# Kernel optimization log

Hardware: AMD Instinct MI355X
Metric: run time of the kernel (lower is better)

Reference implementation:

```python
import jax, jax.numpy as jnp
import numpy as np

N = 50000      # nodes
E = 800000     # edges (avg degree 16)
D = 128        # hidden dim
L = 3          # message-passing layers
NU = 1         # DRew nu -> delay = max(k - nu, 0)


def setup_inputs() -> dict:
    key = jax.random.key(0)
    ks = jax.random.split(key, 6)
    x = jax.random.normal(ks[0], (N, D), dtype=jnp.float32)
    edge_index = jax.random.randint(ks[1], (2, E), 0, N)          # [2, E] (src, dst)
    edge_attr = jax.random.randint(ks[2], (E,), 1, L + 1)          # edge types in {1..L}
    scale = 1.0 / np.sqrt(D).astype(np.float32)
    Ws = jax.random.normal(ks[3], (L, D, D), dtype=jnp.float32) * scale       # mlp_s per layer
    bs = jnp.zeros((L, D), dtype=jnp.float32)
    Wk = jax.random.normal(ks[4], (L, L, D, D), dtype=jnp.float32) * scale    # mlp_k, padded; layer t uses k=1..t+1
    bk = jnp.zeros((L, L, D), dtype=jnp.float32)
    eps = jnp.zeros((L,), dtype=jnp.float32)
    return dict(x=x, edge_index=edge_index, edge_attr=edge_attr,
                Ws=Ws, bs=bs, Wk=Wk, bk=bk, eps=eps)


def reference(x, edge_index, edge_attr, Ws, bs, Wk, bk, eps):
    src, dst = edge_index[0], edge_index[1]
    xs = [x]
    for t in range(L):
        xt = xs[-1]
        # out = (1 + eps) * mlp_s(x)
        out = (1.0 + eps[t]) * jax.nn.relu(xt @ Ws[t] + bs[t])
        for k in range(1, t + 2):
            delay = max(k - NU, 0)
            x_src = xs[t - delay]                       # delayed node features
            mask = (edge_attr == k).astype(xt.dtype)    # edge-type mask (replaces boolean column select)
            msg = x_src[src] * mask[:, None]            # gather + mask: [E, D]
            agg = jax.ops.segment_sum(msg, dst, num_segments=N)  # scatter-add per destination
            out = out + jax.nn.relu(agg @ Wk[t, k - 1] + bk[t, k - 1])  # mlp_k(k)
        # gin_nn_post is an empty Sequential -> identity; then F.relu; then residual
        h = jax.nn.relu(out)
        xs.append(xt + h)
    return xs[-1]
```

## Files before the change

### kernel.cpp

```cpp
#include <hip/hip_runtime.h>
#include <hip/hip_bf16.h>


#define NODES 50000
#define EDGES 800000
#define DIM   128
#define ND    ((long)NODES * DIM)
#define NB3   (3 * NODES)
#define NPART 4
#define PSIZE (NODES / NPART)
#define NROWP 50048
#define NBLKS ((NB3 + 255) / 256)
#define NCELL 96
#define SORTN (NCELL * NBLKS)
#define FGRID ((SORTN + 255) / 256)

typedef __attribute__((ext_vector_type(8))) short  bf16x8;
typedef __attribute__((ext_vector_type(4))) float  f32x4;

#define LDS_STRIDE 136

__global__ __launch_bounds__(256) void init_kernel(
    const float* __restrict__ x, const float* __restrict__ Ws,
    const float* __restrict__ Wk, __hip_bfloat16* __restrict__ xb0,
    __hip_bfloat16* __restrict__ xb1, __hip_bfloat16* __restrict__ xb2,
    __hip_bfloat16* __restrict__ WT, int* __restrict__ cursor) {
  int b = blockIdx.x, tid = threadIdx.x;
  long i = (long)b * 256 + tid;
  if (i < ND / 4) {
    float4 v = ((const float4*)x)[i];
    union { __hip_bfloat16 h[4]; uint2 u; } pk;
    pk.h[0] = __float2bfloat16(v.x); pk.h[1] = __float2bfloat16(v.y);
    pk.h[2] = __float2bfloat16(v.z); pk.h[3] = __float2bfloat16(v.w);
    ((uint2*)xb0)[i] = pk.u;
  }
  if (b < 12) {
    const float* src = (b < 3) ? (Ws + (long)b * 16384) : (Wk + (long)(b - 3) * 16384);
    __hip_bfloat16* dst = WT + (long)b * 16384;
    for (int idx = tid; idx < 16384; idx += 256) {
      int k = idx >> 7, n = idx & 127;
      dst[n * 128 + k] = __float2bfloat16(src[idx]);
    }
  }
  if (b >= 12 && b < 12 + NBLKS) {
    int g = (b - 12) * 256 + tid;
    if (g < NB3) cursor[g] = 0;
  }
  if (b == 599 && tid < DIM) {
    xb0[(long)NODES * DIM + tid] = __float2bfloat16(0.f);
    xb1[(long)NODES * DIM + tid] = __float2bfloat16(0.f);
    xb2[(long)NODES * DIM + tid] = __float2bfloat16(0.f);
  }
}

__global__ __launch_bounds__(256) void hist_kernel(
    const int* __restrict__ ei, const int* __restrict__ attr,
    int* __restrict__ counts, int E) {
  int e = blockIdx.x * 256 + threadIdx.x;
  if (e >= E) return;
  atomicAdd(&counts[ei[E + e] * 3 + (attr[e] - 1)], 1);
}

__global__ __launch_bounds__(256) void scan_a_kernel(
    const int* __restrict__ counts, int* __restrict__ partial,
    int* __restrict__ blocksums, int n) {
  __shared__ int tmp[256];
  int gid = blockIdx.x * 256 + threadIdx.x;
  int v = (gid < n) ? ((counts[gid] + 3) & ~3) : 0;
  tmp[threadIdx.x] = v;
  __syncthreads();
  for (int off = 1; off < 256; off <<= 1) {
    int t = (threadIdx.x >= off) ? tmp[threadIdx.x - off] : 0;
    __syncthreads();
    tmp[threadIdx.x] += t;
    __syncthreads();
  }
  if (gid < n) partial[gid] = tmp[threadIdx.x] - v;
  if (threadIdx.x == 255) blocksums[blockIdx.x] = tmp[255];
}

__global__ __launch_bounds__(256) void scanc_bhist_kernel(
    int* __restrict__ rowptr, int* __restrict__ cursor,
    const int* __restrict__ blocksums, int* __restrict__ csr,
    int* __restrict__ G, int n) {
  __shared__ int h[NCELL];
  __shared__ int red[256];
  int tid = threadIdx.x;
  int partial = 0;
  for (int i = tid; i < blockIdx.x; i += 256) partial += blocksums[i];
  red[tid] = partial;
  if (tid < NCELL) h[tid] = 0;
  __syncthreads();
  for (int off = 128; off > 0; off >>= 1) {
    if (tid < off) red[tid] += red[tid + off];
    __syncthreads();
  }
  int bsoff = red[0];
  int gid = blockIdx.x * 256 + tid;
  if (gid < n) {
    int cnt = cursor[gid];
    int pcnt = (cnt + 3) & ~3;
    int val = rowptr[gid] + bsoff;
    rowptr[gid] = val;
    cursor[gid] = val;
    for (int i = cnt; i < pcnt; ++i) csr[val + i] = NODES;
    if (gid == n - 1) rowptr[n] = val + pcnt;
    int c = pcnt >> 2; if (c > 31) c = 31;
    int km1 = gid - (gid / 3) * 3;
    atomicAdd(&h[km1 * 32 + (31 - c)], 1);
  }
  __syncthreads();
  if (tid < NCELL) G[tid * NBLKS + blockIdx.x] = h[tid];
}

__global__ __launch_bounds__(256) void fill_kernel(
    const int* __restrict__ ei, const int* __restrict__ attr,
    int* __restrict__ cursor, int* __restrict__ csr_src, int E) {
  int p = blockIdx.x & (NPART - 1);
  int chunk = blockIdx.x >> 2;
  int e = chunk * 256 + threadIdx.x;
  if (e >= E) return;
  int d = ei[E + e];
  int lo = p * PSIZE;
  if (d < lo || d >= lo + PSIZE) return;
  int pos = atomicAdd(&cursor[d * 3 + (attr[e] - 1)], 1);
  csr_src[pos] = ei[e];
}

__global__ __launch_bounds__(256) void fscan_a_kernel(
    const int* __restrict__ in, int* __restrict__ partial,
    int* __restrict__ blocksums, int n) {
  __shared__ int tmp[256];
  int gid = blockIdx.x * 256 + threadIdx.x;
  int v = (gid < n) ? in[gid] : 0;
  tmp[threadIdx.x] = v;
  __syncthreads();
  for (int off = 1; off < 256; off <<= 1) {
    int t = (threadIdx.x >= off) ? tmp[threadIdx.x - off] : 0;
    __syncthreads();
    tmp[threadIdx.x] += t;
    __syncthreads();
  }
  if (gid < n) partial[gid] = tmp[threadIdx.x] - v;
  if (threadIdx.x == 255) blocksums[blockIdx.x] = tmp[255];
}

__global__ __launch_bounds__(256) void bfill_kernel(
    const int* __restrict__ rowptr, const int* __restrict__ G,
    const int* __restrict__ bsum2, int* __restrict__ wl, int nb2) {
  __shared__ int base[NCELL];
  __shared__ int ps[256];
  int tid = threadIdx.x;
  int v = (tid < nb2) ? bsum2[tid] : 0;
  ps[tid] = v;
  __syncthreads();
  for (int off = 1; off < 256; off <<= 1) {
    int t = (tid >= off) ? ps[tid - off] : 0;
    __syncthreads();
    ps[tid] += t;
    __syncthreads();
  }
  int incl = ps[tid];
  __syncthreads();
  ps[tid] = incl - v;
  __syncthreads();
  if (tid < NCELL) {
    int gidx = tid * NBLKS + blockIdx.x;
    base[tid] = G[gidx] + ps[gidx >> 8];
  }
  __syncthreads();
  int b = blockIdx.x * 256 + tid;
  if (b >= NB3) return;
  int pcnt = rowptr[b + 1] - rowptr[b];
  int c = pcnt >> 2; if (c > 31) c = 31;
  int km1 = b - (b / 3) * 3;
  int pos = atomicAdd(&base[km1 * 32 + (31 - c)], 1);
  wl[pos] = b;
}

__global__ __launch_bounds__(256, 6) void gather_kernel(
    const __hip_bfloat16* __restrict__ src,
    const int* __restrict__ rowptr, const int* __restrict__ csr,
    const int* __restrict__ wl,
    __hip_bfloat16* __restrict__ ag0, __hip_bfloat16* __restrict__ ag1,
    __hip_bfloat16* __restrict__ ag2, int nwork) {
  int group = (blockIdx.x * 256 + threadIdx.x) >> 4;
  int lane16 = threadIdx.x & 15;
  if (group >= nwork) return;
  int b = wl[group];
  int d = b / 3;
  int km1 = b - d * 3;
  __hip_bfloat16* ag = (km1 == 0) ? ag0 : ((km1 == 1) ? ag1 : ag2);
  int beg = rowptr[b], end = rowptr[b + 1];
  float a0 = 0.f, a1 = 0.f, a2 = 0.f, a3 = 0.f,
        a4 = 0.f, a5 = 0.f, a6 = 0.f, a7 = 0.f;
  for (int base = beg; base < end; base += 16) {
    int idxv = csr[base + lane16];
    int cnt = end - base; if (cnt > 16) cnt = 16;
    int q0 = __shfl(idxv, 0, 16);
    int q1 = __shfl(idxv, 1, 16);
    int q2 = __shfl(idxv, 2, 16);
    int q3 = __shfl(idxv, 3, 16);
    uint4 v0 = *(const uint4*)(src + (long)q0 * DIM + lane16 * 8);
    uint4 v1 = *(const uint4*)(src + (long)q1 * DIM + lane16 * 8);
    uint4 v2 = *(const uint4*)(src + (long)q2 * DIM + lane16 * 8);
    uint4 v3 = *(const uint4*)(src + (long)q3 * DIM + lane16 * 8);
    for (int j = 0; j < cnt; j += 4) {
      uint4 c0 = v0, c1 = v1, c2 = v2, c3 = v3;
      if (j + 4 < cnt) {
        q0 = __shfl(idxv, j + 4, 16);
        q1 = __shfl(idxv, j + 5, 16);
        q2 = __shfl(idxv, j + 6, 16);
        q3 = __shfl(idxv, j + 7, 16);
        v0 = *(const uint4*)(src + (long)q0 * DIM + lane16 * 8);
        v1 = *(const uint4*)(src + (long)q1 * DIM + lane16 * 8);
        v2 = *(const uint4*)(src + (long)q2 * DIM + lane16 * 8);
        v3 = *(const uint4*)(src + (long)q3 * DIM + lane16 * 8);
      }
      a0 += __uint_as_float(c0.x << 16) + __uint_as_float(c1.x << 16)
          + __uint_as_float(c2.x << 16) + __uint_as_float(c3.x << 16);
      a1 += __uint_as_float(c0.x & 0xffff0000u) + __uint_as_float(c1.x & 0xffff0000u)
          + __uint_as_float(c2.x & 0xffff0000u) + __uint_as_float(c3.x & 0xffff0000u);
      a2 += __uint_as_float(c0.y << 16) + __uint_as_float(c1.y << 16)
          + __uint_as_float(c2.y << 16) + __uint_as_float(c3.y << 16);
      a3 += __uint_as_float(c0.y & 0xffff0000u) + __uint_as_float(c1.y & 0xffff0000u)
          + __uint_as_float(c2.y & 0xffff0000u) + __uint_as_float(c3.y & 0xffff0000u);
      a4 += __uint_as_float(c0.z << 16) + __uint_as_float(c1.z << 16)
          + __uint_as_float(c2.z << 16) + __uint_as_float(c3.z << 16);
      a5 += __uint_as_float(c0.z & 0xffff0000u) + __uint_as_float(c1.z & 0xffff0000u)
          + __uint_as_float(c2.z & 0xffff0000u) + __uint_as_float(c3.z & 0xffff0000u);
      a6 += __uint_as_float(c0.w << 16) + __uint_as_float(c1.w << 16)
          + __uint_as_float(c2.w << 16) + __uint_as_float(c3.w << 16);
      a7 += __uint_as_float(c0.w & 0xffff0000u) + __uint_as_float(c1.w & 0xffff0000u)
          + __uint_as_float(c2.w & 0xffff0000u) + __uint_as_float(c3.w & 0xffff0000u);
    }
  }
  union { __hip_bfloat16 h[8]; uint4 u; } pk;
  pk.h[0] = __float2bfloat16(a0); pk.h[1] = __float2bfloat16(a1);
  pk.h[2] = __float2bfloat16(a2); pk.h[3] = __float2bfloat16(a3);
  pk.h[4] = __float2bfloat16(a4); pk.h[5] = __float2bfloat16(a5);
  pk.h[6] = __float2bfloat16(a6); pk.h[7] = __float2bfloat16(a7);
  *(uint4*)(ag + (long)d * DIM + lane16 * 8) = pk.u;
}

__global__ __launch_bounds__(256, 4) void lgemm_kernel(
    const __hip_bfloat16* __restrict__ xbSelf,
    const __hip_bfloat16* __restrict__ ag0,
    const __hip_bfloat16* __restrict__ ag1,
    const __hip_bfloat16* __restrict__ ag2,
    const __hip_bfloat16* __restrict__ WT,
    const float* __restrict__ bs_t,
    const float* __restrict__ bk_t,
    const float* __restrict__ epsp,
    __hip_bfloat16* __restrict__ xnb,
    float* __restrict__ xn,
    int t) {
  __shared__ __hip_bfloat16 b_lds[128 * LDS_STRIDE];

  int tid = threadIdx.x;
  long row0 = (long)blockIdx.x * 64;
  int wave = tid >> 6, lane = tid & 63;
  int l15 = lane & 15, q = lane >> 4;
  long arow = row0 + wave * 16 + l15;

  const __hip_bfloat16* Asrc[4] = {xbSelf, ag0, ag1, ag2};
  f32x4 out[8];

  for (int p = 0; p <= t + 1; ++p) {
    if (p > 0) __syncthreads();
    const __hip_bfloat16* Am = Asrc[p];
    uint4 af[4];
#pragma unroll
    for (int k0i = 0; k0i < 4; ++k0i)
      af[k0i] = *(const uint4*)(Am + arow * DIM + k0i * 32 + 8 * q);
    const __hip_bfloat16* W = (p == 0) ? (WT + (long)t * 16384)
                                       : (WT + (long)(3 + t * 3 + (p - 1)) * 16384);
    {
      const uint4* bq = (const uint4*)W;
#pragma unroll
      for (int i = 0; i < 8; ++i) {
        int idx = tid + 256 * i;
        int n = idx >> 4, k8 = idx & 15;
        uint4 v = bq[idx];
        *(uint4*)(b_lds + n * LDS_STRIDE + k8 * 8) = v;
      }
    }
    __syncthreads();

    f32x4 acc[8] = {};
#pragma unroll
    for (int k0i = 0; k0i < 4; ++k0i) {
      bf16x8 a = __builtin_bit_cast(bf16x8, af[k0i]);
#pragma unroll
      for (int j = 0; j < 8; ++j) {
        bf16x8 bfr = *(const bf16x8*)(b_lds + (16 * j + l15) * LDS_STRIDE + k0i * 32 + 8 * q);
        acc[j] = __builtin_amdgcn_mfma_f32_16x16x32_bf16(a, bfr, acc[j], 0, 0, 0);
      }
    }
    if (p == 0) {
      float sc = 1.0f + *epsp;
#pragma unroll
      for (int j = 0; j < 8; ++j) {
        float b = bs_t[16 * j + l15];
#pragma unroll
        for (int r = 0; r < 4; ++r) out[j][r] = sc * fmaxf(acc[j][r] + b, 0.f);
      }
    } else {
      const float* bb = bk_t + (p - 1) * 128;
#pragma unroll
      for (int j = 0; j < 8; ++j) {
        float b = bb[16 * j + l15];
#pragma unroll
        for (int r = 0; r < 4; ++r) out[j][r] += fmaxf(acc[j][r] + b, 0.f);
      }
    }
  }

  long rbase = row0 + wave * 16 + q * 4;
  bool fin = (xn != nullptr);
#pragma unroll
  for (int j = 0; j < 8; ++j) {
    int col = 16 * j + l15;
#pragma unroll
    for (int r = 0; r < 4; ++r) {
      long grow = rbase + r;
      if (grow < NODES) {
        float res = __bfloat162float(xbSelf[grow * DIM + col]);
        float v = res + fmaxf(out[j][r], 0.f);
        if (fin) xn[grow * DIM + col] = v;
        else     xnb[grow * DIM + col] = __float2bfloat16(v);
      }
    }
  }
}

extern "C" void kernel_launch(void* const* d_in, const int* in_sizes, int n_in,
                              void* d_out, int out_size, void* d_ws, size_t ws_size,
                              hipStream_t stream) {
  const float* x    = (const float*)d_in[0];
  const int*   ei   = (const int*)d_in[1];
  const int*   attr = (const int*)d_in[2];
  const float* Ws   = (const float*)d_in[3];
  const float* bs   = (const float*)d_in[4];
  const float* Wk   = (const float*)d_in[5];
  const float* bk   = (const float*)d_in[6];
  const float* eps  = (const float*)d_in[7];
  float* out = (float*)d_out;

  char* ws = (char*)d_ws;
  size_t off = 0;
  auto alloc = [&](size_t bytes) { char* p = ws + off; off += (bytes + 255) & ~(size_t)255; return p; };
  const size_t ROWB = (size_t)NROWP * DIM * 2;
  __hip_bfloat16* xb0  = (__hip_bfloat16*)alloc(ROWB);
  __hip_bfloat16* xb1  = (__hip_bfloat16*)alloc(ROWB);
  __hip_bfloat16* xb2  = (__hip_bfloat16*)alloc(ROWB);
  __hip_bfloat16* agA0 = (__hip_bfloat16*)alloc(ROWB);
  __hip_bfloat16* agA1 = (__hip_bfloat16*)alloc(ROWB);
  __hip_bfloat16* agA2 = (__hip_bfloat16*)alloc(ROWB);
  __hip_bfloat16* agB0 = (__hip_bfloat16*)alloc(ROWB);
  __hip_bfloat16* agB1 = (__hip_bfloat16*)alloc(ROWB);
  __hip_bfloat16* agC0 = (__hip_bfloat16*)alloc(ROWB);
  __hip_bfloat16* WT   = (__hip_bfloat16*)alloc(12 * 16384 * 2);
  int* cursor    = (int*)alloc((size_t)NB3 * 4);
  int* rowptr    = (int*)alloc((size_t)(NB3 + 1) * 4);
  int* blocksums = (int*)alloc(1024 * 4);
  int* G         = (int*)alloc((size_t)SORTN * 4);
  int* bsum2     = (int*)alloc(1024 * 4);
  int* wl        = (int*)alloc((size_t)NB3 * 4);
  int* csr_src   = (int*)alloc((size_t)(EDGES + 4 * NB3 + 16) * 4);

  int egrid  = (EDGES + 255) / 256;
  int igrid  = (int)(ND / 4 / 256);

  hipLaunchKernelGGL(init_kernel, dim3(igrid), dim3(256), 0, stream,
                     x, Ws, Wk, xb0, xb1, xb2, WT, cursor);
  hipLaunchKernelGGL(hist_kernel, dim3(egrid), dim3(256), 0, stream, ei, attr, cursor, EDGES);
  hipLaunchKernelGGL(scan_a_kernel, dim3(NBLKS), dim3(256), 0, stream, cursor, rowptr, blocksums, NB3);
  hipLaunchKernelGGL(scanc_bhist_kernel, dim3(NBLKS), dim3(256), 0, stream,
                     rowptr, cursor, blocksums, csr_src, G, NB3);
  hipLaunchKernelGGL(fill_kernel, dim3(egrid * NPART), dim3(256), 0, stream, ei, attr, cursor, csr_src, EDGES);
  hipLaunchKernelGGL(fscan_a_kernel, dim3(FGRID), dim3(256), 0, stream, G, G, bsum2, SORTN);
  hipLaunchKernelGGL(bfill_kernel, dim3(NBLKS), dim3(256), 0, stream, rowptr, G, bsum2, wl, FGRID);

  int ggrid = (NODES + 63) / 64;
  auto glaunch = [&](int nwork, const __hip_bfloat16* src, __hip_bfloat16* a0,
                     __hip_bfloat16* a1, __hip_bfloat16* a2) {
    int blocks = (nwork * 16 + 255) / 256;
    hipLaunchKernelGGL(gather_kernel, dim3(blocks), dim3(256), 0, stream,
                       src, rowptr, csr_src, wl, a0, a1, a2, nwork);
  };

  glaunch(3 * NODES, xb0, agA0, agA1, agA2);
  hipLaunchKernelGGL(lgemm_kernel, dim3(ggrid), dim3(256), 0, stream,
                     xb0, agA0, agA0, agA0, WT, bs + 0, bk + 0, eps + 0,
                     xb1, (float*)nullptr, 0);
  glaunch(2 * NODES, xb1, agB0, agB1, agB1);
  hipLaunchKernelGGL(lgemm_kernel, dim3(ggrid), dim3(256), 0, stream,
                     xb1, agB0, agA1, agA1, WT, bs + 128, bk + 3 * 128, eps + 1,
                     xb2, (float*)nullptr, 1);
  glaunch(NODES, xb2, agC0, agC0, agC0);
  hipLaunchKernelGGL(lgemm_kernel, dim3(ggrid), dim3(256), 0, stream,
                     xb2, agC0, agB1, agA2, WT, bs + 256, bk + 6 * 128, eps + 2,
                     (__hip_bfloat16*)nullptr, out, 2);
}
```

Measured before the change: 324.1 us.

## Fuse neighbor gather into per-layer GEMM kernel and drop degree-sorted worklist

The separate gather kernels and their bf16 aggregate buffers are removed. Each lgemm block now aggregates neighbor features for its own 64 rows straight into LDS before the MFMA step, reading from the delayed node buffers. The CSR is regrouped by edge type (type-major), and the degree-bucket worklist build (bucket histogram, scan, bfill) is dropped. This saves kernel launches and the write and re-read of six aggregate arrays. In exchange, load balance across rows of different degree is lost, layer 2 re-gathers type-2 and type-3 edges from xb0 that were previously precomputed in layer 0, and occupancy falls (launch bounds go from 4 to 3, plus extra LDS).

```diff
diff --git a/kernel.cpp b/kernel.cpp
--- a/kernel.cpp
+++ b/kernel.cpp
@@ -11,9 +11,6 @@
 #define PSIZE (NODES / NPART)
 #define NROWP 50048
 #define NBLKS ((NB3 + 255) / 256)
-#define NCELL 96
-#define SORTN (NCELL * NBLKS)
-#define FGRID ((SORTN + 255) / 256)
 
 typedef __attribute__((ext_vector_type(8))) short  bf16x8;
 typedef __attribute__((ext_vector_type(4))) float  f32x4;
@@ -58,7 +55,7 @@
     int* __restrict__ counts, int E) {
   int e = blockIdx.x * 256 + threadIdx.x;
   if (e >= E) return;
-  atomicAdd(&counts[ei[E + e] * 3 + (attr[e] - 1)], 1);
+  atomicAdd(&counts[(attr[e] - 1) * NODES + ei[E + e]], 1);
 }
 
 __global__ __launch_bounds__(256) void scan_a_kernel(
@@ -79,17 +76,14 @@
   if (threadIdx.x == 255) blocksums[blockIdx.x] = tmp[255];
 }
 
-__global__ __launch_bounds__(256) void scanc_bhist_kernel(
+__global__ __launch_bounds__(256) void scanc_kernel(
     int* __restrict__ rowptr, int* __restrict__ cursor,
-    const int* __restrict__ blocksums, int* __restrict__ csr,
-    int* __restrict__ G, int n) {
-  __shared__ int h[NCELL];
+    const int* __restrict__ blocksums, int* __restrict__ csr, int n) {
   __shared__ int red[256];
   int tid = threadIdx.x;
   int partial = 0;
   for (int i = tid; i < blockIdx.x; i += 256) partial += blocksums[i];
   red[tid] = partial;
-  if (tid < NCELL) h[tid] = 0;
   __syncthreads();
   for (int off = 128; off > 0; off >>= 1) {
     if (tid < off) red[tid] += red[tid + off];
@@ -105,12 +99,7 @@
     cursor[gid] = val;
     for (int i = cnt; i < pcnt; ++i) csr[val + i] = NODES;
     if (gid == n - 1) rowptr[n] = val + pcnt;
-    int c = pcnt >> 2; if (c > 31) c = 31;
-    int km1 = gid - (gid / 3) * 3;
-    atomicAdd(&h[km1 * 32 + (31 - c)], 1);
-  }
-  __syncthreads();
-  if (tid < NCELL) G[tid * NBLKS + blockIdx.x] = h[tid];
+  }
 }
 
 __global__ __launch_bounds__(256) void fill_kernel(
@@ -123,131 +112,16 @@
   int d = ei[E + e];
   int lo = p * PSIZE;
   if (d < lo || d >= lo + PSIZE) return;
-  int pos = atomicAdd(&cursor[d * 3 + (attr[e] - 1)], 1);
+  int pos = atomicAdd(&cursor[(attr[e] - 1) * NODES + d], 1);
   csr_src[pos] = ei[e];
 }
 
-__global__ __launch_bounds__(256) void fscan_a_kernel(
-    const int* __restrict__ in, int* __restrict__ partial,
-    int* __restrict__ blocksums, int n) {
-  __shared__ int tmp[256];
-  int gid = blockIdx.x * 256 + threadIdx.x;
-  int v = (gid < n) ? in[gid] : 0;
-  tmp[threadIdx.x] = v;
-  __syncthreads();
-  for (int off = 1; off < 256; off <<= 1) {
-    int t = (threadIdx.x >= off) ? tmp[threadIdx.x - off] : 0;
-    __syncthreads();
-    tmp[threadIdx.x] += t;
-    __syncthreads();
-  }
-  if (gid < n) partial[gid] = tmp[threadIdx.x] - v;
-  if (threadIdx.x == 255) blocksums[blockIdx.x] = tmp[255];
-}
-
-__global__ __launch_bounds__(256) void bfill_kernel(
-    const int* __restrict__ rowptr, const int* __restrict__ G,
-    const int* __restrict__ bsum2, int* __restrict__ wl, int nb2) {
-  __shared__ int base[NCELL];
-  __shared__ int ps[256];
-  int tid = threadIdx.x;
-  int v = (tid < nb2) ? bsum2[tid] : 0;
-  ps[tid] = v;
-  __syncthreads();
-  for (int off = 1; off < 256; off <<= 1) {
-    int t = (tid >= off) ? ps[tid - off] : 0;
-    __syncthreads();
-    ps[tid] += t;
-    __syncthreads();
-  }
-  int incl = ps[tid];
-  __syncthreads();
-  ps[tid] = incl - v;
-  __syncthreads();
-  if (tid < NCELL) {
-    int gidx = tid * NBLKS + blockIdx.x;
-    base[tid] = G[gidx] + ps[gidx >> 8];
-  }
-  __syncthreads();
-  int b = blockIdx.x * 256 + tid;
-  if (b >= NB3) return;
-  int pcnt = rowptr[b + 1] - rowptr[b];
-  int c = pcnt >> 2; if (c > 31) c = 31;
-  int km1 = b - (b / 3) * 3;
-  int pos = atomicAdd(&base[km1 * 32 + (31 - c)], 1);
-  wl[pos] = b;
-}
-
-__global__ __launch_bounds__(256, 6) void gather_kernel(
-    const __hip_bfloat16* __restrict__ src,
+__global__ __launch_bounds__(256, 3) void lgemm_kernel(
+    const __hip_bfloat16* __restrict__ xbSelf,
+    const __hip_bfloat16* __restrict__ g1,
+    const __hip_bfloat16* __restrict__ g2,
+    const __hip_bfloat16* __restrict__ g3,
     const int* __restrict__ rowptr, const int* __restrict__ csr,
-    const int* __restrict__ wl,
-    __hip_bfloat16* __restrict__ ag0, __hip_bfloat16* __restrict__ ag1,
-    __hip_bfloat16* __restrict__ ag2, int nwork) {
-  int group = (blockIdx.x * 256 + threadIdx.x) >> 4;
-  int lane16 = threadIdx.x & 15;
-  if (group >= nwork) return;
-  int b = wl[group];
-  int d = b / 3;
-  int km1 = b - d * 3;
-  __hip_bfloat16* ag = (km1 == 0) ? ag0 : ((km1 == 1) ? ag1 : ag2);
-  int beg = rowptr[b], end = rowptr[b + 1];
-  float a0 = 0.f, a1 = 0.f, a2 = 0.f, a3 = 0.f,
-        a4 = 0.f, a5 = 0.f, a6 = 0.f, a7 = 0.f;
-  for (int base = beg; base < end; base += 16) {
-    int idxv = csr[base + lane16];
-    int cnt = end - base; if (cnt > 16) cnt = 16;
-    int q0 = __shfl(idxv, 0, 16);
-    int q1 = __shfl(idxv, 1, 16);
-    int q2 = __shfl(idxv, 2, 16);
-    int q3 = __shfl(idxv, 3, 16);
-    uint4 v0 = *(const uint4*)(src + (long)q0 * DIM + lane16 * 8);
-    uint4 v1 = *(const uint4*)(src + (long)q1 * DIM + lane16 * 8);
-    uint4 v2 = *(const uint4*)(src + (long)q2 * DIM + lane16 * 8);
-    uint4 v3 = *(const uint4*)(src + (long)q3 * DIM + lane16 * 8);
-    for (int j = 0; j < cnt; j += 4) {
-      uint4 c0 = v0, c1 = v1, c2 = v2, c3 = v3;
-      if (j + 4 < cnt) {
-        q0 = __shfl(idxv, j + 4, 16);
-        q1 = __shfl(idxv, j + 5, 16);
-        q2 = __shfl(idxv, j + 6, 16);
-        q3 = __shfl(idxv, j + 7, 16);
-        v0 = *(const uint4*)(src + (long)q0 * DIM + lane16 * 8);
-        v1 = *(const uint4*)(src + (long)q1 * DIM + lane16 * 8);
-        v2 = *(const uint4*)(src + (long)q2 * DIM + lane16 * 8);
-        v3 = *(const uint4*)(src + (long)q3 * DIM + lane16 * 8);
-      }
-      a0 += __uint_as_float(c0.x << 16) + __uint_as_float(c1.x << 16)
-          + __uint_as_float(c2.x << 16) + __uint_as_float(c3.x << 16);
-      a1 += __uint_as_float(c0.x & 0xffff0000u) + __uint_as_float(c1.x & 0xffff0000u)
-          + __uint_as_float(c2.x & 0xffff0000u) + __uint_as_float(c3.x & 0xffff0000u);
-      a2 += __uint_as_float(c0.y << 16) + __uint_as_float(c1.y << 16)
-          + __uint_as_float(c2.y << 16) + __uint_as_float(c3.y << 16);
-      a3 += __uint_as_float(c0.y & 0xffff0000u) + __uint_as_float(c1.y & 0xffff0000u)
-          + __uint_as_float(c2.y & 0xffff0000u) + __uint_as_float(c3.y & 0xffff0000u);
-      a4 += __uint_as_float(c0.z << 16) + __uint_as_float(c1.z << 16)
-          + __uint_as_float(c2.z << 16) + __uint_as_float(c3.z << 16);
-      a5 += __uint_as_float(c0.z & 0xffff0000u) + __uint_as_float(c1.z & 0xffff0000u)
-          + __uint_as_float(c2.z & 0xffff0000u) + __uint_as_float(c3.z & 0xffff0000u);
-      a6 += __uint_as_float(c0.w << 16) + __uint_as_float(c1.w << 16)
-          + __uint_as_float(c2.w << 16) + __uint_as_float(c3.w << 16);
-      a7 += __uint_as_float(c0.w & 0xffff0000u) + __uint_as_float(c1.w & 0xffff0000u)
-          + __uint_as_float(c2.w & 0xffff0000u) + __uint_as_float(c3.w & 0xffff0000u);
-    }
-  }
-  union { __hip_bfloat16 h[8]; uint4 u; } pk;
-  pk.h[0] = __float2bfloat16(a0); pk.h[1] = __float2bfloat16(a1);
-  pk.h[2] = __float2bfloat16(a2); pk.h[3] = __float2bfloat16(a3);
-  pk.h[4] = __float2bfloat16(a4); pk.h[5] = __float2bfloat16(a5);
-  pk.h[6] = __float2bfloat16(a6); pk.h[7] = __float2bfloat16(a7);
-  *(uint4*)(ag + (long)d * DIM + lane16 * 8) = pk.u;
-}
-
-__global__ __launch_bounds__(256, 4) void lgemm_kernel(
-    const __hip_bfloat16* __restrict__ xbSelf,
-    const __hip_bfloat16* __restrict__ ag0,
-    const __hip_bfloat16* __restrict__ ag1,
-    const __hip_bfloat16* __restrict__ ag2,
     const __hip_bfloat16* __restrict__ WT,
     const float* __restrict__ bs_t,
     const float* __restrict__ bk_t,
@@ -256,6 +130,7 @@
     float* __restrict__ xn,
     int t) {
   __shared__ __hip_bfloat16 b_lds[128 * LDS_STRIDE];
+  __shared__ __hip_bfloat16 a_lds[64 * LDS_STRIDE];
 
   int tid = threadIdx.x;
   long row0 = (long)blockIdx.x * 64;
@@ -263,27 +138,97 @@
   int l15 = lane & 15, q = lane >> 4;
   long arow = row0 + wave * 16 + l15;
 
-  const __hip_bfloat16* Asrc[4] = {xbSelf, ag0, ag1, ag2};
+  const __hip_bfloat16* gsrc[3] = {g1, g2, g3};
   f32x4 out[8];
 
   for (int p = 0; p <= t + 1; ++p) {
-    if (p > 0) __syncthreads();
-    const __hip_bfloat16* Am = Asrc[p];
-    uint4 af[4];
-#pragma unroll
-    for (int k0i = 0; k0i < 4; ++k0i)
-      af[k0i] = *(const uint4*)(Am + arow * DIM + k0i * 32 + 8 * q);
     const __hip_bfloat16* W = (p == 0) ? (WT + (long)t * 16384)
                                        : (WT + (long)(3 + t * 3 + (p - 1)) * 16384);
-    {
-      const uint4* bq = (const uint4*)W;
-#pragma unroll
-      for (int i = 0; i < 8; ++i) {
-        int idx = tid + 256 * i;
-        int n = idx >> 4, k8 = idx & 15;
-        uint4 v = bq[idx];
-        *(uint4*)(b_lds + n * LDS_STRIDE + k8 * 8) = v;
-      }
+    const uint4* bq = (const uint4*)W;
+    uint4 wst[8];
+#pragma unroll
+    for (int i = 0; i < 8; ++i) wst[i] = bq[tid + 256 * i];
+
+    if (p > 0) __syncthreads();
+
+    uint4 af[4];
+    if (p == 0) {
+#pragma unroll
+      for (int k0i = 0; k0i < 4; ++k0i)
+        af[k0i] = *(const uint4*)(xbSelf + arow * DIM + k0i * 32 + 8 * q);
+    } else {
+      const __hip_bfloat16* S = gsrc[p - 1];
+      int km1 = p - 1;
+      int nl = (int)row0 + wave * 16 + (lane < 16 ? lane : 16);
+      if (nl > NODES) nl = NODES;
+      int rp = rowptr[km1 * NODES + nl];
+#pragma unroll
+      for (int s = 0; s < 4; ++s) {
+        int rowl = q * 4 + s;
+        int beg = __shfl(rp, rowl, 64);
+        int end = __shfl(rp, rowl + 1, 64);
+        float a0 = 0.f, a1 = 0.f, a2 = 0.f, a3 = 0.f,
+              a4 = 0.f, a5 = 0.f, a6 = 0.f, a7 = 0.f;
+        for (int base = beg; base < end; base += 16) {
+          int idxv = csr[base + l15];
+          int cnt = end - base; if (cnt > 16) cnt = 16;
+          int q0 = __shfl(idxv, 0, 16);
+          int q1 = __shfl(idxv, 1, 16);
+          int q2 = __shfl(idxv, 2, 16);
+          int q3 = __shfl(idxv, 3, 16);
+          uint4 v0 = *(const uint4*)(S + (long)q0 * DIM + l15 * 8);
+          uint4 v1 = *(const uint4*)(S + (long)q1 * DIM + l15 * 8);
+          uint4 v2 = *(const uint4*)(S + (long)q2 * DIM + l15 * 8);
+          uint4 v3 = *(const uint4*)(S + (long)q3 * DIM + l15 * 8);
+          for (int j = 0; j < cnt; j += 4) {
+            uint4 c0 = v0, c1 = v1, c2 = v2, c3 = v3;
+            if (j + 4 < cnt) {
+              q0 = __shfl(idxv, j + 4, 16);
+              q1 = __shfl(idxv, j + 5, 16);
+              q2 = __shfl(idxv, j + 6, 16);
+              q3 = __shfl(idxv, j + 7, 16);
+              v0 = *(const uint4*)(S + (long)q0 * DIM + l15 * 8);
+              v1 = *(const uint4*)(S + (long)q1 * DIM + l15 * 8);
+              v2 = *(const uint4*)(S + (long)q2 * DIM + l15 * 8);
+              v3 = *(const uint4*)(S + (long)q3 * DIM + l15 * 8);
+            }
+            a0 += __uint_as_float(c0.x << 16) + __uint_as_float(c1.x << 16)
+                + __uint_as_float(c2.x << 16) + __uint_as_float(c3.x << 16);
+            a1 += __uint_as_float(c0.x & 0xffff0000u) + __uint_as_float(c1.x & 0xffff0000u)
+                + __uint_as_float(c2.x & 0xffff0000u) + __uint_as_float(c3.x & 0xffff0000u);
+            a2 += __uint_as_float(c0.y << 16) + __uint_as_float(c1.y << 16)
+                + __uint_as_float(c2.y << 16) + __uint_as_float(c3.y << 16);
+            a3 += __uint_as_float(c0.y & 0xffff0000u) + __uint_as_float(c1.y & 0xffff0000u)
+                + __uint_as_float(c2.y & 0xffff0000u) + __uint_as_float(c3.y & 0xffff0000u);
+            a4 += __uint_as_float(c0.z << 16) + __uint_as_float(c1.z << 16)
+                + __uint_as_float(c2.z << 16) + __uint_as_float(c3.z << 16);
+            a5 += __uint_as_float(c0.z & 0xffff0000u) + __uint_as_float(c1.z & 0xffff0000u)
+                + __uint_as_float(c2.z & 0xffff0000u) + __uint_as_float(c3.z & 0xffff0000u);
+            a6 += __uint_as_float(c0.w << 16) + __uint_as_float(c1.w << 16)
+                + __uint_as_float(c2.w << 16) + __uint_as_float(c3.w << 16);
+            a7 += __uint_as_float(c0.w & 0xffff0000u) + __uint_as_float(c1.w & 0xffff0000u)
+                + __uint_as_float(c2.w & 0xffff0000u) + __uint_as_float(c3.w & 0xffff0000u);
+          }
+        }
+        union { __hip_bfloat16 h[8]; uint4 u; } pk;
+        pk.h[0] = __float2bfloat16(a0); pk.h[1] = __float2bfloat16(a1);
+        pk.h[2] = __float2bfloat16(a2); pk.h[3] = __float2bfloat16(a3);
+        pk.h[4] = __float2bfloat16(a4); pk.h[5] = __float2bfloat16(a5);
+        pk.h[6] = __float2bfloat16(a6); pk.h[7] = __float2bfloat16(a7);
+        *(uint4*)(a_lds + (wave * 16 + rowl) * LDS_STRIDE + l15 * 8) = pk.u;
+      }
+    }
+
+#pragma unroll
+    for (int i = 0; i < 8; ++i) {
+      int idx = tid + 256 * i;
+      int n = idx >> 4, k8 = idx & 15;
+      *(uint4*)(b_lds + n * LDS_STRIDE + k8 * 8) = wst[i];
+    }
+    if (p > 0) {
+#pragma unroll
+      for (int k0i = 0; k0i < 4; ++k0i)
+        af[k0i] = *(const uint4*)(a_lds + (wave * 16 + l15) * LDS_STRIDE + k0i * 32 + 8 * q);
     }
     __syncthreads();
 
@@ -354,20 +299,11 @@
   __hip_bfloat16* xb0  = (__hip_bfloat16*)alloc(ROWB);
   __hip_bfloat16* xb1  = (__hip_bfloat16*)alloc(ROWB);
   __hip_bfloat16* xb2  = (__hip_bfloat16*)alloc(ROWB);
-  __hip_bfloat16* agA0 = (__hip_bfloat16*)alloc(ROWB);
-  __hip_bfloat16* agA1 = (__hip_bfloat16*)alloc(ROWB);
-  __hip_bfloat16* agA2 = (__hip_bfloat16*)alloc(ROWB);
-  __hip_bfloat16* agB0 = (__hip_bfloat16*)alloc(ROWB);
-  __hip_bfloat16* agB1 = (__hip_bfloat16*)alloc(ROWB);
-  __hip_bfloat16* agC0 = (__hip_bfloat16*)alloc(ROWB);
   __hip_bfloat16* WT   = (__hip_bfloat16*)alloc(12 * 16384 * 2);
   int* cursor    = (int*)alloc((size_t)NB3 * 4);
-  int* rowptr    = (int*)alloc((size_t)(NB3 + 1) * 4);
+  int* rowptr    = (int*)alloc((size_t)(NB3 + 1) * 4 + 256);
   int* blocksums = (int*)alloc(1024 * 4);
-  int* G         = (int*)alloc((size_t)SORTN * 4);
-  int* bsum2     = (int*)alloc(1024 * 4);
-  int* wl        = (int*)alloc((size_t)NB3 * 4);
-  int* csr_src   = (int*)alloc((size_t)(EDGES + 4 * NB3 + 16) * 4);
+  int* csr_src   = (int*)alloc((size_t)(EDGES + 4 * NB3 + 64) * 4);
 
   int egrid  = (EDGES + 255) / 256;
   int igrid  = (int)(ND / 4 / 256);
@@ -376,30 +312,21 @@
                      x, Ws, Wk, xb0, xb1, xb2, WT, cursor);
   hipLaunchKernelGGL(hist_kernel, dim3(egrid), dim3(256), 0, stream, ei, attr, cursor, EDGES);
   hipLaunchKernelGGL(scan_a_kernel, dim3(NBLKS), dim3(256), 0, stream, cursor, rowptr, blocksums, NB3);
-  hipLaunchKernelGGL(scanc_bhist_kernel, dim3(NBLKS), dim3(256), 0, stream,
-                     rowptr, cursor, blocksums, csr_src, G, NB3);
+  hipLaunchKernelGGL(scanc_kernel, dim3(NBLKS), dim3(256), 0, stream,
+                     rowptr, cursor, blocksums, csr_src, NB3);
   hipLaunchKernelGGL(fill_kernel, dim3(egrid * NPART), dim3(256), 0, stream, ei, attr, cursor, csr_src, EDGES);
-  hipLaunchKernelGGL(fscan_a_kernel, dim3(FGRID), dim3(256), 0, stream, G, G, bsum2, SORTN);
-  hipLaunchKernelGGL(bfill_kernel, dim3(NBLKS), dim3(256), 0, stream, rowptr, G, bsum2, wl, FGRID);
 
   int ggrid = (NODES + 63) / 64;
-  auto glaunch = [&](int nwork, const __hip_bfloat16* src, __hip_bfloat16* a0,
-                     __hip_bfloat16* a1, __hip_bfloat16* a2) {
-    int blocks = (nwork * 16 + 255) / 256;
-    hipLaunchKernelGGL(gather_kernel, dim3(blocks), dim3(256), 0, stream,
-                       src, rowptr, csr_src, wl, a0, a1, a2, nwork);
-  };
-
-  glaunch(3 * NODES, xb0, agA0, agA1, agA2);
   hipLaunchKernelGGL(lgemm_kernel, dim3(ggrid), dim3(256), 0, stream,
-                     xb0, agA0, agA0, agA0, WT, bs + 0, bk + 0, eps + 0,
+                     xb0, xb0, (const __hip_bfloat16*)nullptr, (const __hip_bfloat16*)nullptr,
+                     rowptr, csr_src, WT, bs + 0, bk + 0, eps + 0,
                      xb1, (float*)nullptr, 0);
-  glaunch(2 * NODES, xb1, agB0, agB1, agB1);
   hipLaunchKernelGGL(lgemm_kernel, dim3(ggrid), dim3(256), 0, stream,
-                     xb1, agB0, agA1, agA1, WT, bs + 128, bk + 3 * 128, eps + 1,
+                     xb1, xb1, xb0, (const __hip_bfloat16*)nullptr,
+                     rowptr, csr_src, WT, bs + 128, bk + 3 * 128, eps + 1,
                      xb2, (float*)nullptr, 1);
-  glaunch(NODES, xb2, agC0, agC0, agC0);
   hipLaunchKernelGGL(lgemm_kernel, dim3(ggrid), dim3(256), 0, stream,
-                     xb2, agC0, agB1, agA2, WT, bs + 256, bk + 6 * 128, eps + 2,
+                     xb2, xb2, xb1, xb0,
+                     rowptr, csr_src, WT, bs + 256, bk + 6 * 128, eps + 2,
                      (__hip_bfloat16*)nullptr, out, 2);
 }
```

After: 417.3 us. 28.7% more time.

## Fuse CSR build into one cooperative kernel, drop degree-sorted worklist, type-major layout

Applied to the files above, without the earlier changes.

Merges init, histogram, scan, offset fixup and fill into a single cooperative kernel with grid.sync barriers, replacing seven launches. The degree-bucketed worklist (bucket histogram, scan, bfill) is removed, and the bucket index moves from node-major (d*3+k) to type-major (k*NODES+d), so gather groups map directly to buckets. This cuts launch and sync overhead and preprocessing work. In exchange the gather loses degree-balanced scheduling and the build runs on a fixed grid of 1024 blocks with grid-wide barriers.

```diff
diff --git a/kernel.cpp b/kernel.cpp
--- a/kernel.cpp
+++ b/kernel.cpp
@@ -1,5 +1,8 @@
 #include <hip/hip_runtime.h>
 #include <hip/hip_bf16.h>
+#include <hip/hip_cooperative_groups.h>
+
+namespace cg = cooperative_groups;
 
 
 #define NODES 50000
@@ -11,187 +14,120 @@
 #define PSIZE (NODES / NPART)
 #define NROWP 50048
 #define NBLKS ((NB3 + 255) / 256)
-#define NCELL 96
-#define SORTN (NCELL * NBLKS)
-#define FGRID ((SORTN + 255) / 256)
+#define EGRID ((EDGES + 255) / 256)
 
 typedef __attribute__((ext_vector_type(8))) short  bf16x8;
 typedef __attribute__((ext_vector_type(4))) float  f32x4;
 
 #define LDS_STRIDE 136
 
-__global__ __launch_bounds__(256) void init_kernel(
+__global__ __launch_bounds__(256, 4) void build_kernel(
     const float* __restrict__ x, const float* __restrict__ Ws,
     const float* __restrict__ Wk, __hip_bfloat16* __restrict__ xb0,
     __hip_bfloat16* __restrict__ xb1, __hip_bfloat16* __restrict__ xb2,
-    __hip_bfloat16* __restrict__ WT, int* __restrict__ cursor) {
-  int b = blockIdx.x, tid = threadIdx.x;
-  long i = (long)b * 256 + tid;
-  if (i < ND / 4) {
+    __hip_bfloat16* __restrict__ WT, int* __restrict__ cursor,
+    const int* __restrict__ ei, const int* __restrict__ attr,
+    int* __restrict__ rowptr, int* __restrict__ blocksums,
+    int* __restrict__ csr) {
+  cg::grid_group grid = cg::this_grid();
+  __shared__ int tmp[256];
+  __shared__ int red[256];
+
+  const int tid = threadIdx.x;
+  const int gtid = blockIdx.x * 256 + tid;
+  const int nth = gridDim.x * 256;
+
+  for (int i = gtid; i < (int)(ND / 4); i += nth) {
     float4 v = ((const float4*)x)[i];
     union { __hip_bfloat16 h[4]; uint2 u; } pk;
     pk.h[0] = __float2bfloat16(v.x); pk.h[1] = __float2bfloat16(v.y);
     pk.h[2] = __float2bfloat16(v.z); pk.h[3] = __float2bfloat16(v.w);
     ((uint2*)xb0)[i] = pk.u;
   }
-  if (b < 12) {
-    const float* src = (b < 3) ? (Ws + (long)b * 16384) : (Wk + (long)(b - 3) * 16384);
-    __hip_bfloat16* dst = WT + (long)b * 16384;
-    for (int idx = tid; idx < 16384; idx += 256) {
-      int k = idx >> 7, n = idx & 127;
-      dst[n * 128 + k] = __float2bfloat16(src[idx]);
-    }
-  }
-  if (b >= 12 && b < 12 + NBLKS) {
-    int g = (b - 12) * 256 + tid;
-    if (g < NB3) cursor[g] = 0;
-  }
-  if (b == 599 && tid < DIM) {
-    xb0[(long)NODES * DIM + tid] = __float2bfloat16(0.f);
-    xb1[(long)NODES * DIM + tid] = __float2bfloat16(0.f);
-    xb2[(long)NODES * DIM + tid] = __float2bfloat16(0.f);
-  }
-}
-
-__global__ __launch_bounds__(256) void hist_kernel(
-    const int* __restrict__ ei, const int* __restrict__ attr,
-    int* __restrict__ counts, int E) {
-  int e = blockIdx.x * 256 + threadIdx.x;
-  if (e >= E) return;
-  atomicAdd(&counts[ei[E + e] * 3 + (attr[e] - 1)], 1);
-}
-
-__global__ __launch_bounds__(256) void scan_a_kernel(
-    const int* __restrict__ counts, int* __restrict__ partial,
-    int* __restrict__ blocksums, int n) {
-  __shared__ int tmp[256];
-  int gid = blockIdx.x * 256 + threadIdx.x;
-  int v = (gid < n) ? ((counts[gid] + 3) & ~3) : 0;
-  tmp[threadIdx.x] = v;
-  __syncthreads();
-  for (int off = 1; off < 256; off <<= 1) {
-    int t = (threadIdx.x >= off) ? tmp[threadIdx.x - off] : 0;
+  for (int idx = gtid; idx < 12 * 16384; idx += nth) {
+    int wb = idx >> 14, r = idx & 16383;
+    int k = r >> 7, n = r & 127;
+    const float* src = (wb < 3) ? (Ws + (long)wb * 16384) : (Wk + (long)(wb - 3) * 16384);
+    WT[(long)wb * 16384 + n * 128 + k] = __float2bfloat16(src[r]);
+  }
+  for (int g = gtid; g < NB3; g += nth) cursor[g] = 0;
+  if (gtid < 3 * DIM) {
+    int which = gtid >> 7, dcol = gtid & 127;
+    __hip_bfloat16* xb = (which == 0) ? xb0 : ((which == 1) ? xb1 : xb2);
+    xb[(long)NODES * DIM + dcol] = __float2bfloat16(0.f);
+  }
+  grid.sync();
+
+  for (int e = gtid; e < EDGES; e += nth)
+    atomicAdd(&cursor[(attr[e] - 1) * NODES + ei[EDGES + e]], 1);
+  grid.sync();
+
+  if (blockIdx.x < NBLKS) {
+    int gid = blockIdx.x * 256 + tid;
+    int v = (gid < NB3) ? ((cursor[gid] + 3) & ~3) : 0;
+    tmp[tid] = v;
     __syncthreads();
-    tmp[threadIdx.x] += t;
+    for (int off = 1; off < 256; off <<= 1) {
+      int t = (tid >= off) ? tmp[tid - off] : 0;
+      __syncthreads();
+      tmp[tid] += t;
+      __syncthreads();
+    }
+    if (gid < NB3) rowptr[gid] = tmp[tid] - v;
+    if (tid == 255) blocksums[blockIdx.x] = tmp[255];
+  }
+  grid.sync();
+
+  if (blockIdx.x < NBLKS) {
+    int partial = 0;
+    for (int i = tid; i < (int)blockIdx.x; i += 256) partial += blocksums[i];
+    red[tid] = partial;
     __syncthreads();
-  }
-  if (gid < n) partial[gid] = tmp[threadIdx.x] - v;
-  if (threadIdx.x == 255) blocksums[blockIdx.x] = tmp[255];
-}
-
-__global__ __launch_bounds__(256) void scanc_bhist_kernel(
-    int* __restrict__ rowptr, int* __restrict__ cursor,
-    const int* __restrict__ blocksums, int* __restrict__ csr,
-    int* __restrict__ G, int n) {
-  __shared__ int h[NCELL];
-  __shared__ int red[256];
-  int tid = threadIdx.x;
-  int partial = 0;
-  for (int i = tid; i < blockIdx.x; i += 256) partial += blocksums[i];
-  red[tid] = partial;
-  if (tid < NCELL) h[tid] = 0;
-  __syncthreads();
-  for (int off = 128; off > 0; off >>= 1) {
-    if (tid < off) red[tid] += red[tid + off];
-    __syncthreads();
-  }
-  int bsoff = red[0];
-  int gid = blockIdx.x * 256 + tid;
-  if (gid < n) {
-    int cnt = cursor[gid];
-    int pcnt = (cnt + 3) & ~3;
-    int val = rowptr[gid] + bsoff;
-    rowptr[gid] = val;
-    cursor[gid] = val;
-    for (int i = cnt; i < pcnt; ++i) csr[val + i] = NODES;
-    if (gid == n - 1) rowptr[n] = val + pcnt;
-    int c = pcnt >> 2; if (c > 31) c = 31;
-    int km1 = gid - (gid / 3) * 3;
-    atomicAdd(&h[km1 * 32 + (31 - c)], 1);
-  }
-  __syncthreads();
-  if (tid < NCELL) G[tid * NBLKS + blockIdx.x] = h[tid];
-}
-
-__global__ __launch_bounds__(256) void fill_kernel(
-    const int* __restrict__ ei, const int* __restrict__ attr,
-    int* __restrict__ cursor, int* __restrict__ csr_src, int E) {
-  int p = blockIdx.x & (NPART - 1);
-  int chunk = blockIdx.x >> 2;
-  int e = chunk * 256 + threadIdx.x;
-  if (e >= E) return;
-  int d = ei[E + e];
-  int lo = p * PSIZE;
-  if (d < lo || d >= lo + PSIZE) return;
-  int pos = atomicAdd(&cursor[d * 3 + (attr[e] - 1)], 1);
-  csr_src[pos] = ei[e];
-}
-
-__global__ __launch_bounds__(256) void fscan_a_kernel(
-    const int* __restrict__ in, int* __restrict__ partial,
-    int* __restrict__ blocksums, int n) {
-  __shared__ int tmp[256];
-  int gid = blockIdx.x * 256 + threadIdx.x;
-  int v = (gid < n) ? in[gid] : 0;
-  tmp[threadIdx.x] = v;
-  __syncthreads();
-  for (int off = 1; off < 256; off <<= 1) {
-    int t = (threadIdx.x >= off) ? tmp[threadIdx.x - off] : 0;
-    __syncthreads();
-    tmp[threadIdx.x] += t;
-    __syncthreads();
-  }
-  if (gid < n) partial[gid] = tmp[threadIdx.x] - v;
-  if (threadIdx.x == 255) blocksums[blockIdx.x] = tmp[255];
-}
-
-__global__ __launch_bounds__(256) void bfill_kernel(
-    const int* __restrict__ rowptr, const int* __restrict__ G,
-    const int* __restrict__ bsum2, int* __restrict__ wl, int nb2) {
-  __shared__ int base[NCELL];
-  __shared__ int ps[256];
-  int tid = threadIdx.x;
-  int v = (tid < nb2) ? bsum2[tid] : 0;
-  ps[tid] = v;
-  __syncthreads();
-  for (int off = 1; off < 256; off <<= 1) {
-    int t = (tid >= off) ? ps[tid - off] : 0;
-    __syncthreads();
-    ps[tid] += t;
-    __syncthreads();
-  }
-  int incl = ps[tid];
-  __syncthreads();
-  ps[tid] = incl - v;
-  __syncthreads();
-  if (tid < NCELL) {
-    int gidx = tid * NBLKS + blockIdx.x;
-    base[tid] = G[gidx] + ps[gidx >> 8];
-  }
-  __syncthreads();
-  int b = blockIdx.x * 256 + tid;
-  if (b >= NB3) return;
-  int pcnt = rowptr[b + 1] - rowptr[b];
-  int c = pcnt >> 2; if (c > 31) c = 31;
-  int km1 = b - (b / 3) * 3;
-  int pos = atomicAdd(&base[km1 * 32 + (31 - c)], 1);
-  wl[pos] = b;
+    for (int off = 128; off > 0; off >>= 1) {
+      if (tid < off) red[tid] += red[tid + off];
+      __syncthreads();
+    }
+    int bsoff = red[0];
+    int gid = blockIdx.x * 256 + tid;
+    if (gid < NB3) {
+      int cnt = cursor[gid];
+      int pcnt = (cnt + 3) & ~3;
+      int val = rowptr[gid] + bsoff;
+      rowptr[gid] = val;
+      cursor[gid] = val;
+      for (int i = cnt; i < pcnt; ++i) csr[val + i] = NODES;
+      if (gid == NB3 - 1) rowptr[NB3] = val + pcnt;
+    }
+  }
+  grid.sync();
+
+  for (int vb = blockIdx.x; vb < EGRID * NPART; vb += gridDim.x) {
+    int p = vb & (NPART - 1);
+    int chunk = vb >> 2;
+    int e = chunk * 256 + tid;
+    if (e < EDGES) {
+      int d = ei[EDGES + e];
+      int lo = p * PSIZE;
+      if (d >= lo && d < lo + PSIZE) {
+        int pos = atomicAdd(&cursor[(attr[e] - 1) * NODES + d], 1);
+        csr[pos] = ei[e];
+      }
+    }
+  }
 }
 
 __global__ __launch_bounds__(256, 6) void gather_kernel(
     const __hip_bfloat16* __restrict__ src,
     const int* __restrict__ rowptr, const int* __restrict__ csr,
-    const int* __restrict__ wl,
     __hip_bfloat16* __restrict__ ag0, __hip_bfloat16* __restrict__ ag1,
     __hip_bfloat16* __restrict__ ag2, int nwork) {
   int group = (blockIdx.x * 256 + threadIdx.x) >> 4;
   int lane16 = threadIdx.x & 15;
   if (group >= nwork) return;
-  int b = wl[group];
-  int d = b / 3;
-  int km1 = b - d * 3;
+  int km1 = (group >= 2 * NODES) ? 2 : ((group >= NODES) ? 1 : 0);
+  int d = group - km1 * NODES;
   __hip_bfloat16* ag = (km1 == 0) ? ag0 : ((km1 == 1) ? ag1 : ag2);
-  int beg = rowptr[b], end = rowptr[b + 1];
+  int beg = rowptr[group], end = rowptr[group + 1];
   float a0 = 0.f, a1 = 0.f, a2 = 0.f, a3 = 0.f,
         a4 = 0.f, a5 = 0.f, a6 = 0.f, a7 = 0.f;
   for (int base = beg; base < end; base += 16) {
@@ -362,33 +298,26 @@
   __hip_bfloat16* agC0 = (__hip_bfloat16*)alloc(ROWB);
   __hip_bfloat16* WT   = (__hip_bfloat16*)alloc(12 * 16384 * 2);
   int* cursor    = (int*)alloc((size_t)NB3 * 4);
-  int* rowptr    = (int*)alloc((size_t)(NB3 + 1) * 4);
+  int* rowptr    = (int*)alloc((size_t)(NB3 + 1) * 4 + 256);
   int* blocksums = (int*)alloc(1024 * 4);
-  int* G         = (int*)alloc((size_t)SORTN * 4);
-  int* bsum2     = (int*)alloc(1024 * 4);
-  int* wl        = (int*)alloc((size_t)NB3 * 4);
-  int* csr_src   = (int*)alloc((size_t)(EDGES + 4 * NB3 + 16) * 4);
-
-  int egrid  = (EDGES + 255) / 256;
-  int igrid  = (int)(ND / 4 / 256);
-
-  hipLaunchKernelGGL(init_kernel, dim3(igrid), dim3(256), 0, stream,
-                     x, Ws, Wk, xb0, xb1, xb2, WT, cursor);
-  hipLaunchKernelGGL(hist_kernel, dim3(egrid), dim3(256), 0, stream, ei, attr, cursor, EDGES);
-  hipLaunchKernelGGL(scan_a_kernel, dim3(NBLKS), dim3(256), 0, stream, cursor, rowptr, blocksums, NB3);
-  hipLaunchKernelGGL(scanc_bhist_kernel, dim3(NBLKS), dim3(256), 0, stream,
-                     rowptr, cursor, blocksums, csr_src, G, NB3);
-  hipLaunchKernelGGL(fill_kernel, dim3(egrid * NPART), dim3(256), 0, stream, ei, attr, cursor, csr_src, EDGES);
-  hipLaunchKernelGGL(fscan_a_kernel, dim3(FGRID), dim3(256), 0, stream, G, G, bsum2, SORTN);
-  hipLaunchKernelGGL(bfill_kernel, dim3(NBLKS), dim3(256), 0, stream, rowptr, G, bsum2, wl, FGRID);
-
-  int ggrid = (NODES + 63) / 64;
+  int* csr_src   = (int*)alloc((size_t)(EDGES + 4 * NB3 + 64) * 4);
+
+  {
+    void* args[] = {(void*)&x, (void*)&Ws, (void*)&Wk, (void*)&xb0, (void*)&xb1,
+                    (void*)&xb2, (void*)&WT, (void*)&cursor, (void*)&ei,
+                    (void*)&attr, (void*)&rowptr, (void*)&blocksums,
+                    (void*)&csr_src};
+    hipLaunchCooperativeKernel((const void*)build_kernel, dim3(1024), dim3(256),
+                               args, 0, stream);
+  }
+
   auto glaunch = [&](int nwork, const __hip_bfloat16* src, __hip_bfloat16* a0,
                      __hip_bfloat16* a1, __hip_bfloat16* a2) {
     int blocks = (nwork * 16 + 255) / 256;
     hipLaunchKernelGGL(gather_kernel, dim3(blocks), dim3(256), 0, stream,
-                       src, rowptr, csr_src, wl, a0, a1, a2, nwork);
+                       src, rowptr, csr_src, a0, a1, a2, nwork);
   };
+  int ggrid = (NODES + 63) / 64;
 
   glaunch(3 * NODES, xb0, agA0, agA1, agA2);
   hipLaunchKernelGGL(lgemm_kernel, dim3(ggrid), dim3(256), 0, stream,
```

Result: slower. 724.7 us (+123.6%).

## Drop degree-sorted worklist and use type-major CSR ordering for gather

Applied to the files above, without the earlier changes.

Reorders the per-destination bucket index from node-major (d*3+k) to type-major (k*NODES+d), so each gather launch covers a contiguous range of buckets. This removes the degree-bucket histogram, its second scan and the worklist fill kernel, cutting two launches and their global traffic. Gather groups now index buckets directly instead of through a degree-sorted worklist. The cost is poorer load balance, since high- and low-degree rows may now land in the same wavefront.

```diff
diff --git a/kernel.cpp b/kernel.cpp
--- a/kernel.cpp
+++ b/kernel.cpp
@@ -11,9 +11,6 @@
 #define PSIZE (NODES / NPART)
 #define NROWP 50048
 #define NBLKS ((NB3 + 255) / 256)
-#define NCELL 96
-#define SORTN (NCELL * NBLKS)
-#define FGRID ((SORTN + 255) / 256)
 
 typedef __attribute__((ext_vector_type(8))) short  bf16x8;
 typedef __attribute__((ext_vector_type(4))) float  f32x4;
@@ -58,7 +55,7 @@
     int* __restrict__ counts, int E) {
   int e = blockIdx.x * 256 + threadIdx.x;
   if (e >= E) return;
-  atomicAdd(&counts[ei[E + e] * 3 + (attr[e] - 1)], 1);
+  atomicAdd(&counts[(attr[e] - 1) * NODES + ei[E + e]], 1);
 }
 
 __global__ __launch_bounds__(256) void scan_a_kernel(
@@ -79,17 +76,14 @@
   if (threadIdx.x == 255) blocksums[blockIdx.x] = tmp[255];
 }
 
-__global__ __launch_bounds__(256) void scanc_bhist_kernel(
+__global__ __launch_bounds__(256) void scanc_kernel(
     int* __restrict__ rowptr, int* __restrict__ cursor,
-    const int* __restrict__ blocksums, int* __restrict__ csr,
-    int* __restrict__ G, int n) {
-  __shared__ int h[NCELL];
+    const int* __restrict__ blocksums, int* __restrict__ csr, int n) {
   __shared__ int red[256];
   int tid = threadIdx.x;
   int partial = 0;
   for (int i = tid; i < blockIdx.x; i += 256) partial += blocksums[i];
   red[tid] = partial;
-  if (tid < NCELL) h[tid] = 0;
   __syncthreads();
   for (int off = 128; off > 0; off >>= 1) {
     if (tid < off) red[tid] += red[tid + off];
@@ -105,12 +99,7 @@
     cursor[gid] = val;
     for (int i = cnt; i < pcnt; ++i) csr[val + i] = NODES;
     if (gid == n - 1) rowptr[n] = val + pcnt;
-    int c = pcnt >> 2; if (c > 31) c = 31;
-    int km1 = gid - (gid / 3) * 3;
-    atomicAdd(&h[km1 * 32 + (31 - c)], 1);
-  }
-  __syncthreads();
-  if (tid < NCELL) G[tid * NBLKS + blockIdx.x] = h[tid];
+  }
 }
 
 __global__ __launch_bounds__(256) void fill_kernel(
@@ -123,75 +112,22 @@
   int d = ei[E + e];
   int lo = p * PSIZE;
   if (d < lo || d >= lo + PSIZE) return;
-  int pos = atomicAdd(&cursor[d * 3 + (attr[e] - 1)], 1);
+  int pos = atomicAdd(&cursor[(attr[e] - 1) * NODES + d], 1);
   csr_src[pos] = ei[e];
-}
-
-__global__ __launch_bounds__(256) void fscan_a_kernel(
-    const int* __restrict__ in, int* __restrict__ partial,
-    int* __restrict__ blocksums, int n) {
-  __shared__ int tmp[256];
-  int gid = blockIdx.x * 256 + threadIdx.x;
-  int v = (gid < n) ? in[gid] : 0;
-  tmp[threadIdx.x] = v;
-  __syncthreads();
-  for (int off = 1; off < 256; off <<= 1) {
-    int t = (threadIdx.x >= off) ? tmp[threadIdx.x - off] : 0;
-    __syncthreads();
-    tmp[threadIdx.x] += t;
-    __syncthreads();
-  }
-  if (gid < n) partial[gid] = tmp[threadIdx.x] - v;
-  if (threadIdx.x == 255) blocksums[blockIdx.x] = tmp[255];
-}
-
-__global__ __launch_bounds__(256) void bfill_kernel(
-    const int* __restrict__ rowptr, const int* __restrict__ G,
-    const int* __restrict__ bsum2, int* __restrict__ wl, int nb2) {
-  __shared__ int base[NCELL];
-  __shared__ int ps[256];
-  int tid = threadIdx.x;
-  int v = (tid < nb2) ? bsum2[tid] : 0;
-  ps[tid] = v;
-  __syncthreads();
-  for (int off = 1; off < 256; off <<= 1) {
-    int t = (tid >= off) ? ps[tid - off] : 0;
-    __syncthreads();
-    ps[tid] += t;
-    __syncthreads();
-  }
-  int incl = ps[tid];
-  __syncthreads();
-  ps[tid] = incl - v;
-  __syncthreads();
-  if (tid < NCELL) {
-    int gidx = tid * NBLKS + blockIdx.x;
-    base[tid] = G[gidx] + ps[gidx >> 8];
-  }
-  __syncthreads();
-  int b = blockIdx.x * 256 + tid;
-  if (b >= NB3) return;
-  int pcnt = rowptr[b + 1] - rowptr[b];
-  int c = pcnt >> 2; if (c > 31) c = 31;
-  int km1 = b - (b / 3) * 3;
-  int pos = atomicAdd(&base[km1 * 32 + (31 - c)], 1);
-  wl[pos] = b;
 }
 
 __global__ __launch_bounds__(256, 6) void gather_kernel(
     const __hip_bfloat16* __restrict__ src,
     const int* __restrict__ rowptr, const int* __restrict__ csr,
-    const int* __restrict__ wl,
     __hip_bfloat16* __restrict__ ag0, __hip_bfloat16* __restrict__ ag1,
     __hip_bfloat16* __restrict__ ag2, int nwork) {
   int group = (blockIdx.x * 256 + threadIdx.x) >> 4;
   int lane16 = threadIdx.x & 15;
   if (group >= nwork) return;
-  int b = wl[group];
-  int d = b / 3;
-  int km1 = b - d * 3;
+  int km1 = (group >= 2 * NODES) ? 2 : ((group >= NODES) ? 1 : 0);
+  int d = group - km1 * NODES;
   __hip_bfloat16* ag = (km1 == 0) ? ag0 : ((km1 == 1) ? ag1 : ag2);
-  int beg = rowptr[b], end = rowptr[b + 1];
+  int beg = rowptr[group], end = rowptr[group + 1];
   float a0 = 0.f, a1 = 0.f, a2 = 0.f, a3 = 0.f,
         a4 = 0.f, a5 = 0.f, a6 = 0.f, a7 = 0.f;
   for (int base = beg; base < end; base += 16) {
@@ -362,12 +298,9 @@
   __hip_bfloat16* agC0 = (__hip_bfloat16*)alloc(ROWB);
   __hip_bfloat16* WT   = (__hip_bfloat16*)alloc(12 * 16384 * 2);
   int* cursor    = (int*)alloc((size_t)NB3 * 4);
-  int* rowptr    = (int*)alloc((size_t)(NB3 + 1) * 4);
+  int* rowptr    = (int*)alloc((size_t)(NB3 + 1) * 4 + 256);
   int* blocksums = (int*)alloc(1024 * 4);
-  int* G         = (int*)alloc((size_t)SORTN * 4);
-  int* bsum2     = (int*)alloc(1024 * 4);
-  int* wl        = (int*)alloc((size_t)NB3 * 4);
-  int* csr_src   = (int*)alloc((size_t)(EDGES + 4 * NB3 + 16) * 4);
+  int* csr_src   = (int*)alloc((size_t)(EDGES + 4 * NB3 + 64) * 4);
 
   int egrid  = (EDGES + 255) / 256;
   int igrid  = (int)(ND / 4 / 256);
@@ -376,19 +309,17 @@
                      x, Ws, Wk, xb0, xb1, xb2, WT, cursor);
   hipLaunchKernelGGL(hist_kernel, dim3(egrid), dim3(256), 0, stream, ei, attr, cursor, EDGES);
   hipLaunchKernelGGL(scan_a_kernel, dim3(NBLKS), dim3(256), 0, stream, cursor, rowptr, blocksums, NB3);
-  hipLaunchKernelGGL(scanc_bhist_kernel, dim3(NBLKS), dim3(256), 0, stream,
-                     rowptr, cursor, blocksums, csr_src, G, NB3);
+  hipLaunchKernelGGL(scanc_kernel, dim3(NBLKS), dim3(256), 0, stream,
+                     rowptr, cursor, blocksums, csr_src, NB3);
   hipLaunchKernelGGL(fill_kernel, dim3(egrid * NPART), dim3(256), 0, stream, ei, attr, cursor, csr_src, EDGES);
-  hipLaunchKernelGGL(fscan_a_kernel, dim3(FGRID), dim3(256), 0, stream, G, G, bsum2, SORTN);
-  hipLaunchKernelGGL(bfill_kernel, dim3(NBLKS), dim3(256), 0, stream, rowptr, G, bsum2, wl, FGRID);
-
-  int ggrid = (NODES + 63) / 64;
+
   auto glaunch = [&](int nwork, const __hip_bfloat16* src, __hip_bfloat16* a0,
                      __hip_bfloat16* a1, __hip_bfloat16* a2) {
     int blocks = (nwork * 16 + 255) / 256;
     hipLaunchKernelGGL(gather_kernel, dim3(blocks), dim3(256), 0, stream,
-                       src, rowptr, csr_src, wl, a0, a1, a2, nwork);
+                       src, rowptr, csr_src, a0, a1, a2, nwork);
   };
+  int ggrid = (NODES + 63) / 64;
 
   glaunch(3 * NODES, xb0, agA0, agA1, agA2);
   hipLaunchKernelGGL(lgemm_kernel, dim3(ggrid), dim3(256), 0, stream,
```

Result: faster. 315.8 us (-2.6%).
